# Optimization experiments

Measured on AMD Instinct MI355X. Metric: run time of the kernel, lower is better.

The kernel has to match this reference:

```python
import jax, jax.numpy as jnp
import numpy as np

N = 10000   # nodes per graph copy
E = 50000   # directed edges before to_undirected
B = 4       # batch size (graph is repeated B times)
K = 16      # num_neg + 1
D = 64      # in_dim == out_dim
R = 200     # num_relation (embedding table has 2R rows)
L = 3       # num_layer
NODE_RATIO = 0.1
DEGREE_RATIO = 1.0


def setup_inputs() -> dict:
    key = jax.random.key(0)
    ks = jax.random.split(key, 16)
    s = 0.05
    edge_index = jax.random.randint(ks[0], (2, E), 0, N, dtype=jnp.int32)
    edge_attr = jax.random.randint(ks[1], (E,), 0, R, dtype=jnp.int32)
    # asserts in source require h and r constant along the negative axis
    h_index = jnp.tile(jax.random.randint(ks[2], (B, 1), 0, N, dtype=jnp.int32), (1, K))
    r_index = jnp.tile(jax.random.randint(ks[3], (B, 1), 0, R, dtype=jnp.int32), (1, K))
    t_index = jax.random.randint(ks[4], (B, K), 0, N, dtype=jnp.int32)
    return {
        'h_index': h_index, 'r_index': r_index, 't_index': t_index,
        'hidden_states': jax.random.normal(ks[5], (B, D), jnp.float32),
        'rel_hidden_states': jax.random.normal(ks[6], (2 * R, D), jnp.float32),
        'edge_index': edge_index, 'edge_attr': edge_attr,
        'score_text_embs': jax.random.normal(ks[7], (N, D), jnp.float32) * 0.1,
        'all_index': jnp.arange(N, dtype=jnp.int32),
        'rel_emb_table': jax.random.normal(ks[8], (2 * R, D), jnp.float32) * s,
        'W_lin': jax.random.normal(ks[9], (2 * D, D), jnp.float32) * s,
        'b_lin': jnp.zeros((D,), jnp.float32),
        'W_mlp1': jax.random.normal(ks[10], (D, 2 * D), jnp.float32) * s,
        'b_mlp1': jnp.zeros((2 * D,), jnp.float32),
        'W_mlp2': jax.random.normal(ks[11], (2 * D, 1), jnp.float32) * s,
        'b_mlp2': jnp.zeros((1,), jnp.float32),
        'rel_w': 1.0 + jax.random.normal(ks[12], (L, 2 * R, D), jnp.float32) * s,
        'conv_W': jax.random.normal(ks[13], (L, 12 * D, D), jnp.float32) * s,
        'conv_b': jnp.zeros((L, D), jnp.float32),
    }


def _score(hidden, rel, W_lin, b_lin, W1, b1, W2, b2):
    # linear(cat[hidden, rel]) -> heuristic; mlp(hidden * heuristic) -> scalar
    heur = jnp.concatenate([hidden, rel], axis=-1) @ W_lin + b_lin
    x = hidden * heur
    h = jax.nn.relu(x @ W1 + b1)
    return (h @ W2 + b2)[..., 0]


def _forward(h_index, r_index, t_index, hidden_states, rel_hidden_states,
             edge_index, edge_attr, score_text_embs, all_index, rel_emb_table,
             W_lin, b_lin, W_mlp1, b_mlp1, W_mlp2, b_mlp2, rel_w, conv_W, conv_b):
    f32 = hidden_states.dtype
    # --- to_undirected: add reversed edges (edge_attr copied, as in PyG) ---
    ei = jnp.concatenate([edge_index, edge_index[::-1]], axis=1)      # [2, 2E]
    ea = jnp.concatenate([edge_attr, edge_attr])                       # [2E]
    E2 = 2 * E
    # --- _repeat_graph: B copies with node-index offsets ---
    offsets = jnp.arange(B, dtype=jnp.int32) * N
    ei_b = jnp.transpose(ei[None] + offsets[:, None, None], (1, 0, 2)).reshape(2, B * E2)
    ea_b = jnp.tile(ea, B)
    Nt, Et = B * N, B * E2
    src, dst = ei_b[0], ei_b[1]
    h0 = h_index[:, 0] + offsets                                       # [B]
    t_full = t_index + offsets[:, None]                                # [B, K]
    rel_embeds = rel_emb_table[r_index[:, 0]].astype(f32)              # [B, D]
    # --- init_input_embeds: tail text embeds then head embeds; score at heads ---
    input_embeds = jnp.zeros((Nt, D), f32).at[all_index].set(score_text_embs)
    input_embeds = input_embeds.at[h0].set(hidden_states)
    score = jnp.zeros((Nt,), f32).at[h0].set(
        _score(hidden_states, rel_embeds, W_lin, b_lin, W_mlp1, b_mlp1, W_mlp2, b_mlp2))
    query0 = rel_embeds[0]   # index_batch is all-zeros in source -> query[0] everywhere
    # --- pna degree mean over the full batched graph ---
    deg_in_full = jax.ops.segment_sum(jnp.ones((Et,), f32), dst, num_segments=Nt)
    pna_mean = jnp.mean(jnp.log(deg_in_full + 1.0))
    ks_n = max(1, int(NODE_RATIO * Nt))
    es = max(1, int(DEGREE_RATIO * ks_n * Et / Nt))
    hidden = input_embeds
    for l in range(L):
        # select_edges: top-ks nodes by score, then top-es outgoing edges
        thr = jax.lax.top_k(score, ks_n)[0][-1]
        s_src = score[src]
        edge_score = jnp.where(s_src >= thr, s_src, -jnp.inf)
        thr_e = jax.lax.top_k(edge_score, es)[0][-1]
        emask = (edge_score >= thr_e) & jnp.isfinite(edge_score)       # [Et]
        em = emask.astype(f32)
        # relation-conditioned messages gated by sigmoid(score of source)
        m = jax.nn.sigmoid(s_src)[:, None] * hidden[src] * rel_w[l][ea_b]
        mf = m * em[:, None]
        deg = jax.ops.segment_sum(em, dst, num_segments=Nt)            # [Nt]
        denom = jnp.maximum(deg, 1.0)[:, None]
        mean_a = jax.ops.segment_sum(mf, dst, num_segments=Nt) / denom
        sq = jax.ops.segment_sum(mf * mf, dst, num_segments=Nt) / denom
        std = jnp.sqrt(jnp.maximum(sq - mean_a * mean_a, 0.0) + 1e-6)
        mmax = jax.ops.segment_max(jnp.where(emask[:, None], m, -jnp.inf), dst, num_segments=Nt)
        mmin = jax.ops.segment_min(jnp.where(emask[:, None], m, jnp.inf), dst, num_segments=Nt)
        has = (deg > 0)[:, None]
        mmax = jnp.where(has, mmax, 0.0)
        mmin = jnp.where(has, mmin, 0.0)
        feat = jnp.concatenate([mean_a, mmax, mmin, std], axis=-1)     # [Nt, 4D]
        sc_log = jnp.log(deg + 1.0)
        amp = (sc_log / pna_mean)[:, None]
        att = (pna_mean / (sc_log + 1e-6))[:, None]
        feat_all = jnp.concatenate([feat, feat * amp, feat * att], -1)  # [Nt, 12D]
        upd = jax.nn.relu(feat_all @ conv_W[l] + conv_b[l])            # [Nt, D]
        out_deg = jax.ops.segment_sum(em, src, num_segments=Nt)
        omask = out_deg > 0
        hidden = jnp.where(omask[:, None], hidden + upd, hidden)
        new_score = _score(hidden, jnp.broadcast_to(query0, hidden.shape),
                           W_lin, b_lin, W_mlp1, b_mlp1, W_mlp2, b_mlp2)
        score = jnp.where(omask, new_score, score)
    return score[t_full]                                               # [B, K]


def reference(h_index, r_index, t_index, hidden_states, rel_hidden_states,
              edge_index, edge_attr, score_text_embs, all_index, rel_emb_table,
              W_lin, b_lin, W_mlp1, b_mlp1, W_mlp2, b_mlp2, rel_w, conv_W, conv_b):
    return _forward(h_index, r_index, t_index, hidden_states, rel_hidden_states,
                    edge_index, edge_attr, score_text_embs, all_index, rel_emb_table,
                    W_lin, b_lin, W_mlp1, b_mlp1, W_mlp2, b_mlp2, rel_w, conv_W, conv_b)
```

## Files before the change

### kernel.cpp

```cpp
#include <hip/hip_runtime.h>
#include <math.h>

#define N_NODES 10000
#define E_EDGES 50000
#define NT      40000
#define KS_N    4000
#define ES_E    40000
#define WTOT    400000u
#define CHUNK   16384
#define SEL_BLOCKS 40

__device__ __forceinline__ unsigned f2u(float f) {
    unsigned b = __float_as_uint(f);
    return (b & 0x80000000u) ? ~b : (b | 0x80000000u);
}
__device__ __forceinline__ float u2f(unsigned u) {
    unsigned b = (u & 0x80000000u) ? (u & 0x7fffffffu) : ~u;
    return __uint_as_float(b);
}
__device__ __forceinline__ float wave_sum64(float x) {
    for (int off = 32; off > 0; off >>= 1) x += __shfl_down(x, off, 64);
    return x;
}

__global__ void count_deg(const int* __restrict__ ei, unsigned* __restrict__ deg) {
    int j = blockIdx.x * 256 + threadIdx.x;
    if (j < E_EDGES) {
        atomicAdd(&deg[ei[j]], 1u);
        atomicAdd(&deg[ei[E_EDGES + j]], 1u);
    }
}

__global__ __launch_bounds__(1024) void scan_degrees(const unsigned* __restrict__ deg,
                                                     unsigned* __restrict__ rowptr,
                                                     unsigned* __restrict__ cursor) {
    __shared__ unsigned wsum[16];
    __shared__ unsigned carry;
    int tid = threadIdx.x, lane = tid & 63, w = tid >> 6;
    if (tid == 0) carry = 0;
    __syncthreads();
    for (int base = 0; base < N_NODES; base += 1024) {
        int i = base + tid;
        unsigned v = (i < N_NODES) ? deg[i] : 0u;
        unsigned x = v;
        for (int off = 1; off < 64; off <<= 1) {
            unsigned y = __shfl_up(x, off, 64);
            if (lane >= off) x += y;
        }
        if (lane == 63) wsum[w] = x;
        __syncthreads();
        if (tid < 16) {
            unsigned s = wsum[tid];
            for (int off = 1; off < 16; off <<= 1) {
                unsigned y = __shfl_up(s, off, 64);
                if (tid >= off) s += y;
            }
            wsum[tid] = s;
        }
        __syncthreads();
        unsigned woff = (w > 0) ? wsum[w - 1] : 0u;
        unsigned excl = carry + woff + x - v;
        if (i < N_NODES) { rowptr[i] = excl; cursor[i] = excl; }
        __syncthreads();
        if (tid == 0) carry += wsum[15];
        __syncthreads();
    }
    if (tid == 0) rowptr[N_NODES] = carry;
}

__global__ void scatter_edges(const int* __restrict__ ei, const int* __restrict__ ea,
                              unsigned* __restrict__ cursor, unsigned* __restrict__ inedge) {
    int j = blockIdx.x * 256 + threadIdx.x;
    if (j < E_EDGES) {
        unsigned s = (unsigned)ei[j];
        unsigned d = (unsigned)ei[E_EDGES + j];
        unsigned a = (unsigned)ea[j];
        unsigned p1 = atomicAdd(&cursor[d], 1u);
        inedge[p1] = s | (a << 16);
        unsigned p2 = atomicAdd(&cursor[s], 1u);
        inedge[p2] = d | (a << 16);
    }
}

__global__ __launch_bounds__(1024) void pna_kernel(const unsigned* __restrict__ degb,
                                                   float* __restrict__ scalars) {
    __shared__ float ws[16];
    int tid = threadIdx.x;
    float s = 0.0f;
    for (int i = tid; i < N_NODES; i += 1024) s += logf((float)degb[i] + 1.0f);
    for (int off = 32; off > 0; off >>= 1) s += __shfl_down(s, off, 64);
    if ((tid & 63) == 0) ws[tid >> 6] = s;
    __syncthreads();
    if (tid == 0) {
        float t = 0.0f;
        for (int i = 0; i < 16; ++i) t += ws[i];
        scalars[3] = t / (float)N_NODES;
    }
}

__global__ void init_hidden(const float* __restrict__ text, float* __restrict__ hidden) {
    int i = blockIdx.x * 256 + threadIdx.x;
    if (i < NT * 64) {
        int v = i >> 6;
        hidden[i] = (v < N_NODES) ? text[i] : 0.0f;
    }
}

__device__ float wave_score_g(float hid, float rel, const float* Wlin, const float* blin,
                              const float* W1, const float* b1, const float* W2, float b2v,
                              int lane) {
    float heur = blin[lane];
    for (int i = 0; i < 64; ++i) heur += __shfl(hid, i, 64) * Wlin[i * 64 + lane];
    for (int i = 0; i < 64; ++i) heur += __shfl(rel, i, 64) * Wlin[(64 + i) * 64 + lane];
    float x = hid * heur;
    float a0 = b1[lane], a1 = b1[64 + lane];
    for (int i = 0; i < 64; ++i) {
        float xv = __shfl(x, i, 64);
        a0 += xv * W1[i * 128 + lane];
        a1 += xv * W1[i * 128 + 64 + lane];
    }
    a0 = fmaxf(a0, 0.0f); a1 = fmaxf(a1, 0.0f);
    float part = a0 * W2[lane] + a1 * W2[64 + lane];
    part = wave_sum64(part);
    part = __shfl(part, 0, 64);
    return part + b2v;
}

__global__ void init_heads(const int* __restrict__ h_index, const int* __restrict__ r_index,
                           const float* __restrict__ hidden_states,
                           const float* __restrict__ rel_table,
                           const float* __restrict__ W_lin, const float* __restrict__ b_lin,
                           const float* __restrict__ W1, const float* __restrict__ b1,
                           const float* __restrict__ W2, const float* __restrict__ b2,
                           float* __restrict__ hidden, float* __restrict__ score,
                           float* __restrict__ qh) {
    __shared__ float q0[64];
    int tid = threadIdx.x, w = tid >> 6, lane = tid & 63;
    int b = w;
    int h0 = h_index[b * 16] + b * N_NODES;
    float hs  = hidden_states[b * 64 + lane];
    float rel = rel_table[r_index[b * 16] * 64 + lane];
    hidden[h0 * 64 + lane] = hs;
    if (b == 0) q0[lane] = rel;
    float s = wave_score_g(hs, rel, W_lin, b_lin, W1, b1, W2, b2[0], lane);
    if (lane == 0) score[h0] = s;
    __syncthreads();
    if (w == 0) {
        float acc = b_lin[lane];
        for (int i = 0; i < 64; ++i) acc += q0[i] * W_lin[(64 + i) * 64 + lane];
        qh[lane] = acc;
    }
}

__device__ void block_pick(unsigned h, unsigned r, unsigned* outd, unsigned* outr,
                           unsigned* scr) {
    int tid = threadIdx.x, lane = tid & 63, w = tid >> 6;
    __syncthreads();
    unsigned x = h;
    for (int off = 1; off < 64; off <<= 1) {
        unsigned y = __shfl_up(x, off, 64);
        if (lane >= off) x += y;
    }
    if (lane == 63) scr[w] = x;
    __syncthreads();
    unsigned woff = 0;
    for (int i = 0; i < 4; ++i) if (i < w) woff += scr[i];
    unsigned excl = woff + x - h;
    if (r >= excl && r < excl + h) { scr[4] = (unsigned)tid; scr[5] = r - excl; }
    __syncthreads();
    *outd = scr[4]; *outr = scr[5];
}

__global__ __launch_bounds__(256) void select_compact(
    const float* __restrict__ score, const unsigned* __restrict__ degb,
    unsigned* __restrict__ ghn, unsigned* __restrict__ ghw,
    unsigned* __restrict__ state, float* __restrict__ scalars,
    unsigned* __restrict__ countp, int* __restrict__ list,
    float* __restrict__ sigp, int rbase) {
    __shared__ unsigned lh[512];
    __shared__ unsigned scr[8];
    __shared__ unsigned sh_flag;
    __shared__ unsigned sh_state[4];
    int tid = threadIdx.x;
    unsigned pn = 0, pw = 0;
    unsigned rn = NT - KS_N, rw_ = WTOT - ES_E;
    for (int pass = 0; pass < 4; ++pass) {
        lh[tid] = 0; lh[256 + tid] = 0;
        __syncthreads();
        int shift = 24 - pass * 8;
        for (int v = blockIdx.x * 256 + tid; v < NT; v += SEL_BLOCKS * 256) {
            unsigned key = f2u(score[v]);
            unsigned wg = degb[v % N_NODES];
            unsigned dig = (key >> shift) & 255u;
            if (pass == 0) {
                atomicAdd(&lh[dig], 1u);
                if (wg) atomicAdd(&lh[256 + dig], wg);
            } else {
                unsigned hi = key >> (shift + 8);
                if (hi == pn) atomicAdd(&lh[dig], 1u);
                if (wg && hi == pw) atomicAdd(&lh[256 + dig], wg);
            }
        }
        __syncthreads();
        if (lh[tid]) atomicAdd(&ghn[tid], lh[tid]);
        if (lh[256 + tid]) atomicAdd(&ghw[tid], lh[256 + tid]);
        __threadfence();
        __syncthreads();
        if (tid == 0)
            sh_flag = (atomicAdd(&state[8], 1u) == SEL_BLOCKS - 1) ? 1u : 0u;
        __syncthreads();
        unsigned tgt = (unsigned)(rbase + pass + 1);
        if (sh_flag) {
            unsigned hn = atomicAdd(&ghn[tid], 0u);
            unsigned hw = atomicAdd(&ghw[tid], 0u);
            ghn[tid] = 0; ghw[tid] = 0;
            unsigned dn, rn2, dw, rw2;
            block_pick(hn, rn, &dn, &rn2, scr);
            block_pick(hw, rw_, &dw, &rw2, scr);
            if (tid == 0) {
                pn = (pn << 8) | dn;
                pw = (pw << 8) | dw;
                state[0] = pn; state[1] = rn2; state[2] = pw; state[3] = rw2;
                state[8] = 0;
                if (pass == 3) {
                    float thr = u2f(pn), thre = u2f(pw);
                    scalars[0] = thr;
                    scalars[1] = fmaxf(thr, thre);
                    *countp = 0;
                }
                __threadfence();
                atomicExch(&state[9], tgt);
            }
        }
        if (tid == 0) {
            while (atomicAdd(&state[9], 0u) < tgt) __builtin_amdgcn_s_sleep(8);
            sh_state[0] = atomicAdd(&state[0], 0u);
            sh_state[1] = atomicAdd(&state[1], 0u);
            sh_state[2] = atomicAdd(&state[2], 0u);
            sh_state[3] = atomicAdd(&state[3], 0u);
        }
        __syncthreads();
        pn = sh_state[0]; rn = sh_state[1]; pw = sh_state[2]; rw_ = sh_state[3];
    }
    float thr = u2f(pn);
    float THR = fmaxf(thr, u2f(pw));
    for (int v = blockIdx.x * 256 + tid; v < NT; v += SEL_BLOCKS * 256) {
        float sc = score[v];
        bool ok = sc >= THR;
        float sg = -1.0f;
        if (ok) sg = 1.0f / (1.0f + expf(-sc));
        sigp[v] = sg;
        if (ok && degb[v % N_NODES] > 0) {
            unsigned p = atomicAdd(countp, 1u);
            list[p] = v;
        }
    }
}

__global__ __launch_bounds__(256) void agg_feat(
    const float* __restrict__ sigp, const float* __restrict__ hidden,
    const unsigned* __restrict__ rowptr, const unsigned* __restrict__ inedge,
    const float* __restrict__ rel_w, const float* __restrict__ scalars,
    const unsigned* __restrict__ countp, const int* __restrict__ list,
    float* __restrict__ feat, float* __restrict__ ampatt, int layer,
    int mbase, int climit) {
    int count = (int)*countp;
    int cc = count - mbase; if (cc > climit) cc = climit;
    int tid = threadIdx.x, w = tid >> 6, lane = tid & 63;
    int li = blockIdx.x * 4 + w;
    if (li >= cc) return;
    int v = list[mbase + li];
    int b = v / N_NODES;
    int boff = b * N_NODES;
    int n = v - boff;
    const float* rw = rel_w + (size_t)layer * 400 * 64;
    unsigned r0 = rowptr[n], r1 = rowptr[n + 1];
    float sum = 0.f, sq = 0.f, mx = -INFINITY, mn = INFINITY;
    int cnt = 0;
    #pragma unroll 2
    for (unsigned e = r0; e < r1; ++e) {
        unsigned pk = inedge[e];
        int src = (int)(pk & 0xffffu) + boff;
        float sg = sigp[src];
        float h  = hidden[((size_t)src << 6) + lane];
        float rv = rw[((size_t)(pk >> 16) << 6) + lane];
        bool valid = sg >= 0.0f;
        float mval = sg * h * rv;
        if (valid) { sum += mval; sq += mval * mval; }
        mx = fmaxf(mx, valid ? mval : -INFINITY);
        mn = fminf(mn, valid ? mval : INFINITY);
        cnt += valid ? 1 : 0;
    }
    float denom = cnt > 0 ? (float)cnt : 1.0f;
    float mean = sum / denom;
    float sd = sqrtf(fmaxf(sq / denom - mean * mean, 0.0f) + 1e-6f);
    float* fr = feat + ((size_t)li << 8);
    fr[lane]        = mean;
    fr[64 + lane]   = cnt > 0 ? mx : 0.0f;
    fr[128 + lane]  = cnt > 0 ? mn : 0.0f;
    fr[192 + lane]  = sd;
    if (lane == 0) {
        float pna = scalars[3];
        float sl = logf((float)cnt + 1.0f);
        ampatt[li * 2]     = sl / pna;
        ampatt[li * 2 + 1] = pna / (sl + 1e-6f);
    }
}

#define FMA4(C, av, bv) { C[0] += av * bv.x; C[1] += av * bv.y; C[2] += av * bv.z; C[3] += av * bv.w; }

__global__ __launch_bounds__(256) void gemm_upd(
    const float* __restrict__ conv_W, const float* __restrict__ conv_b,
    const unsigned* __restrict__ countp, const float* __restrict__ feat,
    const float* __restrict__ ampatt, float* __restrict__ updc,
    int layer, int mbase, int climit) {
    __shared__ float sA[32][68];
    __shared__ float sB[32][196];
    __shared__ float sAmp[64], sAtt[64];
    int count = (int)*countp;
    int cc = count - mbase; if (cc > climit) cc = climit;
    int m0 = blockIdx.x * 64;
    if (m0 >= cc) return;
    int tid = threadIdx.x;
    if (tid < 64) {
        int rl = m0 + tid;
        float a = 0.f, t = 0.f;
        if (rl < cc) { a = ampatt[rl * 2]; t = ampatt[rl * 2 + 1]; }
        sAmp[tid] = a; sAtt[tid] = t;
    }
    int mg = tid >> 4, ng = tid & 15;
    int j0 = ng * 4;
    float c0[4][4] = {}, c1[4][4] = {}, c2[4][4] = {};
    const float* Wl = conv_W + (size_t)layer * 768 * 64;
    const float4* feat4 = (const float4*)feat;
    for (int k0 = 0; k0 < 256; k0 += 32) {
        __syncthreads();
        #pragma unroll
        for (int it = 0; it < 2; ++it) {
            int fi = it * 256 + tid;
            int arow = fi >> 3, akq = fi & 7;
            float4 va = feat4[(((size_t)(m0 + arow)) << 6) + (k0 >> 2) + akq];
            sA[akq * 4 + 0][arow] = va.x; sA[akq * 4 + 1][arow] = va.y;
            sA[akq * 4 + 2][arow] = va.z; sA[akq * 4 + 3][arow] = va.w;
        }
        #pragma unroll
        for (int it = 0; it < 6; ++it) {
            int fi = it * 256 + tid;
            int rr = fi >> 4, q = fi & 15;
            int part = rr >> 5, kk = rr & 31;
            float4 vb = *(const float4*)(Wl + (((size_t)(part * 256 + k0 + kk)) << 6) + q * 4);
            float* d = &sB[kk][part * 64 + q * 4];
            d[0] = vb.x; d[1] = vb.y; d[2] = vb.z; d[3] = vb.w;
        }
        __syncthreads();
        #pragma unroll 4
        for (int kk = 0; kk < 32; ++kk) {
            float4 a  = *(const float4*)&sA[kk][mg * 4];
            float4 b0 = *(const float4*)&sB[kk][j0];
            float4 b1 = *(const float4*)&sB[kk][64 + j0];
            float4 b2 = *(const float4*)&sB[kk][128 + j0];
            FMA4(c0[0], a.x, b0) FMA4(c0[1], a.y, b0) FMA4(c0[2], a.z, b0) FMA4(c0[3], a.w, b0)
            FMA4(c1[0], a.x, b1) FMA4(c1[1], a.y, b1) FMA4(c1[2], a.z, b1) FMA4(c1[3], a.w, b1)
            FMA4(c2[0], a.x, b2) FMA4(c2[1], a.y, b2) FMA4(c2[2], a.z, b2) FMA4(c2[3], a.w, b2)
        }
    }
    const float4 bias = *(const float4*)(conv_b + layer * 64 + j0);
    #pragma unroll
    for (int mi = 0; mi < 4; ++mi) {
        int ml = mg * 4 + mi;
        int rl = m0 + ml;
        if (rl < cc) {
            float amp = sAmp[ml], att = sAtt[ml];
            float4 o;
            o.x = fmaxf(c0[mi][0] + amp * c1[mi][0] + att * c2[mi][0] + bias.x, 0.0f);
            o.y = fmaxf(c0[mi][1] + amp * c1[mi][1] + att * c2[mi][1] + bias.y, 0.0f);
            o.z = fmaxf(c0[mi][2] + amp * c1[mi][2] + att * c2[mi][2] + bias.z, 0.0f);
            o.w = fmaxf(c0[mi][3] + amp * c1[mi][3] + att * c2[mi][3] + bias.w, 0.0f);
            *(float4*)(updc + (((size_t)(mbase + rl)) << 6) + j0) = o;
        }
    }
}

__global__ __launch_bounds__(256) void apply_score_gemm(
    float* __restrict__ hidden, const float* __restrict__ updc,
    float* __restrict__ score, const unsigned* __restrict__ countp,
    const int* __restrict__ list,
    const float* __restrict__ W_lin, const float* __restrict__ qh,
    const float* __restrict__ W1, const float* __restrict__ b1,
    const float* __restrict__ W2, const float* __restrict__ b2) {
    __shared__ float sH[64][65];
    __shared__ float sX[64][65];
    int count = (int)*countp;
    int m0 = blockIdx.x * 64;
    if (m0 >= count) return;
    int tid = threadIdx.x;

    {
        int q = tid & 15;
        int mB = tid >> 4;
        #pragma unroll
        for (int r = 0; r < 4; ++r) {
            int m = r * 16 + mB;
            int idx = m0 + m;
            float4 hv = {0.f, 0.f, 0.f, 0.f};
            if (idx < count) {
                int v = list[idx];
                hv = *(const float4*)&hidden[((size_t)v << 6) + q * 4];
                float4 uv = *(const float4*)&updc[((size_t)idx << 6) + q * 4];
                hv.x += uv.x; hv.y += uv.y; hv.z += uv.z; hv.w += uv.w;
                *(float4*)&hidden[((size_t)v << 6) + q * 4] = hv;
            }
            sH[m][q * 4 + 0] = hv.x; sH[m][q * 4 + 1] = hv.y;
            sH[m][q * 4 + 2] = hv.z; sH[m][q * 4 + 3] = hv.w;
        }
    }
    __syncthreads();

    int mg = tid >> 4, ng = tid & 15;
    const float4* Wl4 = (const float4*)W_lin;
    const float4* W14 = (const float4*)W1;
    const float4* qh4 = (const float4*)qh;
    const float4* b14 = (const float4*)b1;
    const float4* W24 = (const float4*)W2;

    {
        float4 qv = qh4[ng];
        float acc[4][4];
        #pragma unroll
        for (int mi = 0; mi < 4; ++mi) {
            acc[mi][0] = qv.x; acc[mi][1] = qv.y; acc[mi][2] = qv.z; acc[mi][3] = qv.w;
        }
        for (int k = 0; k < 64; ++k) {
            float4 bv = Wl4[k * 16 + ng];
            #pragma unroll
            for (int mi = 0; mi < 4; ++mi) {
                float av = sH[mg * 4 + mi][k];
                acc[mi][0] += av * bv.x; acc[mi][1] += av * bv.y;
                acc[mi][2] += av * bv.z; acc[mi][3] += av * bv.w;
            }
        }
        #pragma unroll
        for (int mi = 0; mi < 4; ++mi) {
            int m = mg * 4 + mi;
            #pragma unroll
            for (int ni = 0; ni < 4; ++ni)
                sX[m][ng * 4 + ni] = sH[m][ng * 4 + ni] * acc[mi][ni];
        }
    }
    __syncthreads();

    {
        float4 bA = b14[ng], bB = b14[16 + ng];
        float accA[4][4], accB[4][4];
        #pragma unroll
        for (int mi = 0; mi < 4; ++mi) {
            accA[mi][0] = bA.x; accA[mi][1] = bA.y; accA[mi][2] = bA.z; accA[mi][3] = bA.w;
            accB[mi][0] = bB.x; accB[mi][1] = bB.y; accB[mi][2] = bB.z; accB[mi][3] = bB.w;
        }
        for (int k = 0; k < 64; ++k) {
            float4 bvA = W14[k * 32 + ng];
            float4 bvB = W14[k * 32 + 16 + ng];
            #pragma unroll
            for (int mi = 0; mi < 4; ++mi) {
                float av = sX[mg * 4 + mi][k];
                accA[mi][0] += av * bvA.x; accA[mi][1] += av * bvA.y;
                accA[mi][2] += av * bvA.z; accA[mi][3] += av * bvA.w;
                accB[mi][0] += av * bvB.x; accB[mi][1] += av * bvB.y;
                accB[mi][2] += av * bvB.z; accB[mi][3] += av * bvB.w;
            }
        }
        float4 w2A = W24[ng], w2B = W24[16 + ng];
        #pragma unroll
        for (int mi = 0; mi < 4; ++mi) {
            int m = mg * 4 + mi;
            float pA0 = fmaxf(accA[mi][0], 0.f), pB0 = fmaxf(accB[mi][0], 0.f);
            float pA1 = fmaxf(accA[mi][1], 0.f), pB1 = fmaxf(accB[mi][1], 0.f);
            float pA2 = fmaxf(accA[mi][2], 0.f), pB2 = fmaxf(accB[mi][2], 0.f);
            float pA3 = fmaxf(accA[mi][3], 0.f), pB3 = fmaxf(accB[mi][3], 0.f);
            sH[m][ng * 4 + 0] = pA0 * w2A.x + pB0 * w2B.x;
            sH[m][ng * 4 + 1] = pA1 * w2A.y + pB1 * w2B.y;
            sH[m][ng * 4 + 2] = pA2 * w2A.z + pB2 * w2B.z;
            sH[m][ng * 4 + 3] = pA3 * w2A.w + pB3 * w2B.w;
        }
    }
    __syncthreads();

    {
        float b2v = b2[0];
        int w = tid >> 6, lane = tid & 63;
        #pragma unroll 4
        for (int t = 0; t < 16; ++t) {
            int m = w * 16 + t;
            float p = sH[m][lane];
            float s = wave_sum64(p);
            if (lane == 0) {
                int idx = m0 + m;
                if (idx < count) score[list[idx]] = s + b2v;
            }
        }
    }
}

__global__ void gather_out(const float* __restrict__ score, const int* __restrict__ t_index,
                           float* __restrict__ out) {
    int i = threadIdx.x;
    int b = i >> 4;
    out[i] = score[t_index[i] + b * N_NODES];
}

extern "C" void kernel_launch(void* const* d_in, const int* in_sizes, int n_in,
                              void* d_out, int out_size, void* d_ws, size_t ws_size,
                              hipStream_t stream) {
    const int*   h_index       = (const int*)d_in[0];
    const int*   r_index       = (const int*)d_in[1];
    const int*   t_index       = (const int*)d_in[2];
    const float* hidden_states = (const float*)d_in[3];
    const int*   edge_index    = (const int*)d_in[5];
    const int*   edge_attr     = (const int*)d_in[6];
    const float* text          = (const float*)d_in[7];
    const float* rel_table     = (const float*)d_in[9];
    const float* W_lin         = (const float*)d_in[10];
    const float* b_lin         = (const float*)d_in[11];
    const float* W1            = (const float*)d_in[12];
    const float* b1            = (const float*)d_in[13];
    const float* W2            = (const float*)d_in[14];
    const float* b2            = (const float*)d_in[15];
    const float* rel_w         = (const float*)d_in[16];
    const float* conv_W        = (const float*)d_in[17];
    const float* conv_b        = (const float*)d_in[18];

    auto layout_bytes = [](size_t fch) -> size_t {
        auto al = [](size_t x) { return (x + 255) & ~(size_t)255; };
        size_t o = 0;
        o += al(256) * 3;
        o += al(1024) * 2;
        o += al((size_t)NT * 4);
        o += al((size_t)N_NODES * 4);
        o += al(256);
        o += al((size_t)NT * 4);
        o += al((size_t)NT * 64 * 4);
        o += al((size_t)NT * 64 * 4);
        o += al(fch * 256 * 4);
        o += al(fch * 2 * 4);
        o += al((size_t)NT * 4);
        o += al((size_t)(N_NODES + 1) * 4);
        o += al((size_t)N_NODES * 4);
        o += al((size_t)2 * E_EDGES * 4);
        return o;
    };
    const size_t FCH = (layout_bytes(NT) <= ws_size) ? (size_t)NT : (size_t)CHUNK;
    const int NCH = (FCH == (size_t)NT) ? 1 : 3;

    char* ws = (char*)d_ws;
    size_t off = 0;
    auto carve = [&](size_t bytes) -> char* {
        char* p = ws + off;
        off = (off + bytes + 255) & ~(size_t)255;
        return p;
    };
    float*    scalars = (float*)carve(256);
    unsigned* state   = (unsigned*)carve(256);
    unsigned* countp  = (unsigned*)carve(256);
    unsigned* ghn     = (unsigned*)carve(1024);
    unsigned* ghw     = (unsigned*)carve(1024);
    float*    score   = (float*)carve((size_t)NT * 4);
    unsigned* degb    = (unsigned*)carve((size_t)N_NODES * 4);
    size_t zero_end = off;
    float*    qh      = (float*)carve(256);
    float*    sigp    = (float*)carve((size_t)NT * 4);
    float*    hidden  = (float*)carve((size_t)NT * 64 * 4);
    float*    updc    = (float*)carve((size_t)NT * 64 * 4);
    float*    feat    = (float*)carve(FCH * 256 * 4);
    float*    ampatt  = (float*)carve(FCH * 2 * 4);
    int*      list    = (int*)carve((size_t)NT * 4);
    unsigned* rowptr  = (unsigned*)carve((size_t)(N_NODES + 1) * 4);
    unsigned* cursor  = (unsigned*)carve((size_t)N_NODES * 4);
    unsigned* inedge  = (unsigned*)carve((size_t)2 * E_EDGES * 4);
    if (off > ws_size) return;

    hipMemsetAsync(ws, 0, zero_end, stream);

    count_deg<<<(E_EDGES + 255) / 256, 256, 0, stream>>>(edge_index, degb);
    scan_degrees<<<1, 1024, 0, stream>>>(degb, rowptr, cursor);
    scatter_edges<<<(E_EDGES + 255) / 256, 256, 0, stream>>>(edge_index, edge_attr, cursor, inedge);
    pna_kernel<<<1, 1024, 0, stream>>>(degb, scalars);
    init_hidden<<<(NT * 64 + 255) / 256, 256, 0, stream>>>(text, hidden);
    init_heads<<<1, 256, 0, stream>>>(h_index, r_index, hidden_states, rel_table,
                                      W_lin, b_lin, W1, b1, W2, b2, hidden, score, qh);

    const int climit  = (int)FCH;
    const int aggGrid = climit / 4;
    const int gemGrid = climit / 64;
    for (int l = 0; l < 3; ++l) {
        select_compact<<<SEL_BLOCKS, 256, 0, stream>>>(score, degb, ghn, ghw, state,
                                                       scalars, countp, list, sigp, l * 4);
        for (int c = 0; c < NCH; ++c) {
            int mbase = c * climit;
            agg_feat<<<aggGrid, 256, 0, stream>>>(sigp, hidden, rowptr, inedge, rel_w,
                                                  scalars, countp, list, feat, ampatt,
                                                  l, mbase, climit);
            gemm_upd<<<gemGrid, 256, 0, stream>>>(conv_W, conv_b, countp, feat, ampatt,
                                                  updc, l, mbase, climit);
        }
        apply_score_gemm<<<(NT + 63) / 64, 256, 0, stream>>>(hidden, updc, score, countp,
                                                             list, W_lin, qh, W1, b1, W2, b2);
    }
    gather_out<<<1, 64, 0, stream>>>(score, t_index, (float*)d_out);
}
```

Before: 466.5 us.

## Fuse conv update GEMM with hidden apply and score MLP per tile

Merges the per-layer conv update GEMM and the apply/score kernel into one kernel that keeps the update tile in shared memory, adds it to hidden, and computes the score MLP in place. This removes the updc intermediate buffer, its global write and read, and one launch per layer. The tile height drops from 64 to 32 rows so the merged kernel's shared memory and registers fit, which doubles the number of blocks but lowers reuse of the streamed weights per block. Hidden updates now happen per chunk inside the chunk loop rather than after all chunks.

```diff
diff --git a/kernel.cpp b/kernel.cpp
--- a/kernel.cpp
+++ b/kernel.cpp
@@ -309,39 +309,44 @@
 
 #define FMA4(C, av, bv) { C[0] += av * bv.x; C[1] += av * bv.y; C[2] += av * bv.z; C[3] += av * bv.w; }
 
-__global__ __launch_bounds__(256) void gemm_upd(
+__global__ __launch_bounds__(256) void update_score(
     const float* __restrict__ conv_W, const float* __restrict__ conv_b,
     const unsigned* __restrict__ countp, const float* __restrict__ feat,
-    const float* __restrict__ ampatt, float* __restrict__ updc,
+    const float* __restrict__ ampatt, float* __restrict__ hidden,
+    float* __restrict__ score, const int* __restrict__ list,
+    const float* __restrict__ W_lin, const float* __restrict__ qh,
+    const float* __restrict__ W1, const float* __restrict__ b1,
+    const float* __restrict__ W2, const float* __restrict__ b2,
     int layer, int mbase, int climit) {
-    __shared__ float sA[32][68];
-    __shared__ float sB[32][196];
-    __shared__ float sAmp[64], sAtt[64];
+    __shared__ float smem[32 * 34 + 32 * 196 + 64];
+    float* sA   = smem;
+    float* sB   = smem + 32 * 34;
+    float* sAmp = smem + 32 * 34 + 32 * 196;
+    float* sAtt = sAmp + 32;
     int count = (int)*countp;
     int cc = count - mbase; if (cc > climit) cc = climit;
-    int m0 = blockIdx.x * 64;
+    int m0 = blockIdx.x * 32;
     if (m0 >= cc) return;
     int tid = threadIdx.x;
-    if (tid < 64) {
+    if (tid < 32) {
         int rl = m0 + tid;
         float a = 0.f, t = 0.f;
         if (rl < cc) { a = ampatt[rl * 2]; t = ampatt[rl * 2 + 1]; }
         sAmp[tid] = a; sAtt[tid] = t;
     }
-    int mg = tid >> 4, ng = tid & 15;
-    int j0 = ng * 4;
-    float c0[4][4] = {}, c1[4][4] = {}, c2[4][4] = {};
+    int mg = tid >> 4, ng = tid & 15, j0 = ng * 4;
+    float c0[2][4] = {}, c1[2][4] = {}, c2[2][4] = {};
     const float* Wl = conv_W + (size_t)layer * 768 * 64;
     const float4* feat4 = (const float4*)feat;
+    int arow = tid >> 3, akq = tid & 7;
     for (int k0 = 0; k0 < 256; k0 += 32) {
         __syncthreads();
-        #pragma unroll
-        for (int it = 0; it < 2; ++it) {
-            int fi = it * 256 + tid;
-            int arow = fi >> 3, akq = fi & 7;
+        {
             float4 va = feat4[(((size_t)(m0 + arow)) << 6) + (k0 >> 2) + akq];
-            sA[akq * 4 + 0][arow] = va.x; sA[akq * 4 + 1][arow] = va.y;
-            sA[akq * 4 + 2][arow] = va.z; sA[akq * 4 + 3][arow] = va.w;
+            sA[(akq * 4 + 0) * 34 + arow] = va.x;
+            sA[(akq * 4 + 1) * 34 + arow] = va.y;
+            sA[(akq * 4 + 2) * 34 + arow] = va.z;
+            sA[(akq * 4 + 3) * 34 + arow] = va.w;
         }
         #pragma unroll
         for (int it = 0; it < 6; ++it) {
@@ -349,111 +354,99 @@
             int rr = fi >> 4, q = fi & 15;
             int part = rr >> 5, kk = rr & 31;
             float4 vb = *(const float4*)(Wl + (((size_t)(part * 256 + k0 + kk)) << 6) + q * 4);
-            float* d = &sB[kk][part * 64 + q * 4];
+            float* d = &sB[kk * 196 + part * 64 + q * 4];
             d[0] = vb.x; d[1] = vb.y; d[2] = vb.z; d[3] = vb.w;
         }
         __syncthreads();
         #pragma unroll 4
         for (int kk = 0; kk < 32; ++kk) {
-            float4 a  = *(const float4*)&sA[kk][mg * 4];
-            float4 b0 = *(const float4*)&sB[kk][j0];
-            float4 b1 = *(const float4*)&sB[kk][64 + j0];
-            float4 b2 = *(const float4*)&sB[kk][128 + j0];
-            FMA4(c0[0], a.x, b0) FMA4(c0[1], a.y, b0) FMA4(c0[2], a.z, b0) FMA4(c0[3], a.w, b0)
-            FMA4(c1[0], a.x, b1) FMA4(c1[1], a.y, b1) FMA4(c1[2], a.z, b1) FMA4(c1[3], a.w, b1)
-            FMA4(c2[0], a.x, b2) FMA4(c2[1], a.y, b2) FMA4(c2[2], a.z, b2) FMA4(c2[3], a.w, b2)
+            float a0 = sA[kk * 34 + mg * 2];
+            float a1 = sA[kk * 34 + mg * 2 + 1];
+            float4 b0 = *(const float4*)&sB[kk * 196 + j0];
+            float4 b1v = *(const float4*)&sB[kk * 196 + 64 + j0];
+            float4 b2v = *(const float4*)&sB[kk * 196 + 128 + j0];
+            FMA4(c0[0], a0, b0)  FMA4(c0[1], a1, b0)
+            FMA4(c1[0], a0, b1v) FMA4(c1[1], a1, b1v)
+            FMA4(c2[0], a0, b2v) FMA4(c2[1], a1, b2v)
         }
     }
     const float4 bias = *(const float4*)(conv_b + layer * 64 + j0);
+    float4 o[2];
     #pragma unroll
-    for (int mi = 0; mi < 4; ++mi) {
-        int ml = mg * 4 + mi;
-        int rl = m0 + ml;
-        if (rl < cc) {
-            float amp = sAmp[ml], att = sAtt[ml];
-            float4 o;
-            o.x = fmaxf(c0[mi][0] + amp * c1[mi][0] + att * c2[mi][0] + bias.x, 0.0f);
-            o.y = fmaxf(c0[mi][1] + amp * c1[mi][1] + att * c2[mi][1] + bias.y, 0.0f);
-            o.z = fmaxf(c0[mi][2] + amp * c1[mi][2] + att * c2[mi][2] + bias.z, 0.0f);
-            o.w = fmaxf(c0[mi][3] + amp * c1[mi][3] + att * c2[mi][3] + bias.w, 0.0f);
-            *(float4*)(updc + (((size_t)(mbase + rl)) << 6) + j0) = o;
-        }
-    }
-}
-
-__global__ __launch_bounds__(256) void apply_score_gemm(
-    float* __restrict__ hidden, const float* __restrict__ updc,
-    float* __restrict__ score, const unsigned* __restrict__ countp,
-    const int* __restrict__ list,
-    const float* __restrict__ W_lin, const float* __restrict__ qh,
-    const float* __restrict__ W1, const float* __restrict__ b1,
-    const float* __restrict__ W2, const float* __restrict__ b2) {
-    __shared__ float sH[64][65];
-    __shared__ float sX[64][65];
-    int count = (int)*countp;
-    int m0 = blockIdx.x * 64;
-    if (m0 >= count) return;
-    int tid = threadIdx.x;
-
+    for (int mi = 0; mi < 2; ++mi) {
+        int ml = mg * 2 + mi;
+        float amp = sAmp[ml], att = sAtt[ml];
+        o[mi].x = fmaxf(c0[mi][0] + amp * c1[mi][0] + att * c2[mi][0] + bias.x, 0.0f);
+        o[mi].y = fmaxf(c0[mi][1] + amp * c1[mi][1] + att * c2[mi][1] + bias.y, 0.0f);
+        o[mi].z = fmaxf(c0[mi][2] + amp * c1[mi][2] + att * c2[mi][2] + bias.z, 0.0f);
+        o[mi].w = fmaxf(c0[mi][3] + amp * c1[mi][3] + att * c2[mi][3] + bias.w, 0.0f);
+    }
+    __syncthreads();
+    float* sH = smem;
+    float* sX = smem + 32 * 65;
+    #pragma unroll
+    for (int mi = 0; mi < 2; ++mi) {
+        int ml = mg * 2 + mi;
+        sH[ml * 65 + j0 + 0] = o[mi].x; sH[ml * 65 + j0 + 1] = o[mi].y;
+        sH[ml * 65 + j0 + 2] = o[mi].z; sH[ml * 65 + j0 + 3] = o[mi].w;
+    }
+    __syncthreads();
     {
-        int q = tid & 15;
-        int mB = tid >> 4;
+        int q = tid & 15, mB = tid >> 4;
         #pragma unroll
-        for (int r = 0; r < 4; ++r) {
+        for (int r = 0; r < 2; ++r) {
             int m = r * 16 + mB;
             int idx = m0 + m;
-            float4 hv = {0.f, 0.f, 0.f, 0.f};
-            if (idx < count) {
-                int v = list[idx];
-                hv = *(const float4*)&hidden[((size_t)v << 6) + q * 4];
-                float4 uv = *(const float4*)&updc[((size_t)idx << 6) + q * 4];
-                hv.x += uv.x; hv.y += uv.y; hv.z += uv.z; hv.w += uv.w;
-                *(float4*)&hidden[((size_t)v << 6) + q * 4] = hv;
+            if (idx < cc) {
+                int v = list[mbase + idx];
+                float4 hv = *(const float4*)&hidden[((size_t)v << 6) + q * 4];
+                float h0 = hv.x + sH[m * 65 + q * 4 + 0];
+                float h1 = hv.y + sH[m * 65 + q * 4 + 1];
+                float h2 = hv.z + sH[m * 65 + q * 4 + 2];
+                float h3 = hv.w + sH[m * 65 + q * 4 + 3];
+                float4 hw = {h0, h1, h2, h3};
+                *(float4*)&hidden[((size_t)v << 6) + q * 4] = hw;
+                sH[m * 65 + q * 4 + 0] = h0; sH[m * 65 + q * 4 + 1] = h1;
+                sH[m * 65 + q * 4 + 2] = h2; sH[m * 65 + q * 4 + 3] = h3;
+            } else {
+                sH[m * 65 + q * 4 + 0] = 0.f; sH[m * 65 + q * 4 + 1] = 0.f;
+                sH[m * 65 + q * 4 + 2] = 0.f; sH[m * 65 + q * 4 + 3] = 0.f;
             }
-            sH[m][q * 4 + 0] = hv.x; sH[m][q * 4 + 1] = hv.y;
-            sH[m][q * 4 + 2] = hv.z; sH[m][q * 4 + 3] = hv.w;
-        }
-    }
-    __syncthreads();
-
-    int mg = tid >> 4, ng = tid & 15;
+        }
+    }
+    __syncthreads();
     const float4* Wl4 = (const float4*)W_lin;
     const float4* W14 = (const float4*)W1;
-    const float4* qh4 = (const float4*)qh;
-    const float4* b14 = (const float4*)b1;
-    const float4* W24 = (const float4*)W2;
-
     {
-        float4 qv = qh4[ng];
-        float acc[4][4];
+        float4 qv = ((const float4*)qh)[ng];
+        float acc[2][4];
         #pragma unroll
-        for (int mi = 0; mi < 4; ++mi) {
+        for (int mi = 0; mi < 2; ++mi) {
             acc[mi][0] = qv.x; acc[mi][1] = qv.y; acc[mi][2] = qv.z; acc[mi][3] = qv.w;
         }
         for (int k = 0; k < 64; ++k) {
             float4 bv = Wl4[k * 16 + ng];
             #pragma unroll
-            for (int mi = 0; mi < 4; ++mi) {
-                float av = sH[mg * 4 + mi][k];
+            for (int mi = 0; mi < 2; ++mi) {
+                float av = sH[(mg * 2 + mi) * 65 + k];
                 acc[mi][0] += av * bv.x; acc[mi][1] += av * bv.y;
                 acc[mi][2] += av * bv.z; acc[mi][3] += av * bv.w;
             }
         }
         #pragma unroll
-        for (int mi = 0; mi < 4; ++mi) {
-            int m = mg * 4 + mi;
+        for (int mi = 0; mi < 2; ++mi) {
+            int m = mg * 2 + mi;
             #pragma unroll
             for (int ni = 0; ni < 4; ++ni)
-                sX[m][ng * 4 + ni] = sH[m][ng * 4 + ni] * acc[mi][ni];
-        }
-    }
-    __syncthreads();
-
+                sX[m * 65 + j0 + ni] = sH[m * 65 + j0 + ni] * acc[mi][ni];
+        }
+    }
+    __syncthreads();
     {
-        float4 bA = b14[ng], bB = b14[16 + ng];
-        float accA[4][4], accB[4][4];
+        float4 bA = ((const float4*)b1)[ng], bB = ((const float4*)b1)[16 + ng];
+        float accA[2][4], accB[2][4];
         #pragma unroll
-        for (int mi = 0; mi < 4; ++mi) {
+        for (int mi = 0; mi < 2; ++mi) {
             accA[mi][0] = bA.x; accA[mi][1] = bA.y; accA[mi][2] = bA.z; accA[mi][3] = bA.w;
             accB[mi][0] = bB.x; accB[mi][1] = bB.y; accB[mi][2] = bB.z; accB[mi][3] = bB.w;
         }
@@ -461,42 +454,39 @@
             float4 bvA = W14[k * 32 + ng];
             float4 bvB = W14[k * 32 + 16 + ng];
             #pragma unroll
-            for (int mi = 0; mi < 4; ++mi) {
-                float av = sX[mg * 4 + mi][k];
+            for (int mi = 0; mi < 2; ++mi) {
+                float av = sX[(mg * 2 + mi) * 65 + k];
                 accA[mi][0] += av * bvA.x; accA[mi][1] += av * bvA.y;
                 accA[mi][2] += av * bvA.z; accA[mi][3] += av * bvA.w;
                 accB[mi][0] += av * bvB.x; accB[mi][1] += av * bvB.y;
                 accB[mi][2] += av * bvB.z; accB[mi][3] += av * bvB.w;
             }
         }
-        float4 w2A = W24[ng], w2B = W24[16 + ng];
+        float4 w2A = ((const float4*)W2)[ng], w2B = ((const float4*)W2)[16 + ng];
         #pragma unroll
-        for (int mi = 0; mi < 4; ++mi) {
-            int m = mg * 4 + mi;
+        for (int mi = 0; mi < 2; ++mi) {
+            int m = mg * 2 + mi;
             float pA0 = fmaxf(accA[mi][0], 0.f), pB0 = fmaxf(accB[mi][0], 0.f);
             float pA1 = fmaxf(accA[mi][1], 0.f), pB1 = fmaxf(accB[mi][1], 0.f);
             float pA2 = fmaxf(accA[mi][2], 0.f), pB2 = fmaxf(accB[mi][2], 0.f);
             float pA3 = fmaxf(accA[mi][3], 0.f), pB3 = fmaxf(accB[mi][3], 0.f);
-            sH[m][ng * 4 + 0] = pA0 * w2A.x + pB0 * w2B.x;
-            sH[m][ng * 4 + 1] = pA1 * w2A.y + pB1 * w2B.y;
-            sH[m][ng * 4 + 2] = pA2 * w2A.z + pB2 * w2B.z;
-            sH[m][ng * 4 + 3] = pA3 * w2A.w + pB3 * w2B.w;
-        }
-    }
-    __syncthreads();
-
+            sH[m * 65 + j0 + 0] = pA0 * w2A.x + pB0 * w2B.x;
+            sH[m * 65 + j0 + 1] = pA1 * w2A.y + pB1 * w2B.y;
+            sH[m * 65 + j0 + 2] = pA2 * w2A.z + pB2 * w2B.z;
+            sH[m * 65 + j0 + 3] = pA3 * w2A.w + pB3 * w2B.w;
+        }
+    }
+    __syncthreads();
     {
         float b2v = b2[0];
         int w = tid >> 6, lane = tid & 63;
         #pragma unroll 4
-        for (int t = 0; t < 16; ++t) {
-            int m = w * 16 + t;
-            float p = sH[m][lane];
+        for (int t = 0; t < 8; ++t) {
+            int m = w * 8 + t;
+            float p = sH[m * 65 + lane];
             float s = wave_sum64(p);
-            if (lane == 0) {
-                int idx = m0 + m;
-                if (idx < count) score[list[idx]] = s + b2v;
-            }
+            if (lane == 0 && (m0 + m) < cc)
+                score[list[mbase + m0 + m]] = s + b2v;
         }
     }
 }
@@ -539,7 +529,6 @@
         o += al(256);
         o += al((size_t)NT * 4);
         o += al((size_t)NT * 64 * 4);
-        o += al((size_t)NT * 64 * 4);
         o += al(fch * 256 * 4);
         o += al(fch * 2 * 4);
         o += al((size_t)NT * 4);
@@ -569,7 +558,6 @@
     float*    qh      = (float*)carve(256);
     float*    sigp    = (float*)carve((size_t)NT * 4);
     float*    hidden  = (float*)carve((size_t)NT * 64 * 4);
-    float*    updc    = (float*)carve((size_t)NT * 64 * 4);
     float*    feat    = (float*)carve(FCH * 256 * 4);
     float*    ampatt  = (float*)carve(FCH * 2 * 4);
     int*      list    = (int*)carve((size_t)NT * 4);
@@ -590,7 +578,7 @@
 
     const int climit  = (int)FCH;
     const int aggGrid = climit / 4;
-    const int gemGrid = climit / 64;
+    const int updGrid = climit / 32;
     for (int l = 0; l < 3; ++l) {
         select_compact<<<SEL_BLOCKS, 256, 0, stream>>>(score, degb, ghn, ghw, state,
                                                        scalars, countp, list, sigp, l * 4);
@@ -599,11 +587,10 @@
             agg_feat<<<aggGrid, 256, 0, stream>>>(sigp, hidden, rowptr, inedge, rel_w,
                                                   scalars, countp, list, feat, ampatt,
                                                   l, mbase, climit);
-            gemm_upd<<<gemGrid, 256, 0, stream>>>(conv_W, conv_b, countp, feat, ampatt,
-                                                  updc, l, mbase, climit);
-        }
-        apply_score_gemm<<<(NT + 63) / 64, 256, 0, stream>>>(hidden, updc, score, countp,
-                                                             list, W_lin, qh, W1, b1, W2, b2);
+            update_score<<<updGrid, 256, 0, stream>>>(conv_W, conv_b, countp, feat, ampatt,
+                                                      hidden, score, list, W_lin, qh,
+                                                      W1, b1, W2, b2, l, mbase, climit);
+        }
     }
     gather_out<<<1, 64, 0, stream>>>(score, t_index, (float*)d_out);
 }
```

Measured after the change: 397.2 us, median of 3. 1.17x faster.
